# Optimization experiments

Hardware: AMD Instinct MI355X
Metric: run time of the kernel (lower is better)

## Reference

```python
import jax, jax.numpy as jnp
import numpy as np

EMBED_DIM = 32
HIDDEN_DIM = 16

def _xavier(key, fan_in, fan_out):
    limit = float(np.sqrt(6.0 / (fan_in + fan_out)))
    return jax.random.uniform(key, (fan_in, fan_out), jnp.float32, -limit, limit)

def setup_inputs() -> dict:
    key = jax.random.key(0)
    ks = jax.random.split(key, 7)
    N = 1_000_000
    H = jax.random.normal(ks[0], (N, EMBED_DIM), jnp.float32)
    TPL = jax.random.normal(ks[1], (1, 1), jnp.float32)
    # params (xavier-uniform weights, zero biases, matching torch init)
    Wv = _xavier(ks[2], EMBED_DIM, HIDDEN_DIM); bv = jnp.zeros((HIDDEN_DIM,), jnp.float32)
    Wu = _xavier(ks[3], EMBED_DIM, HIDDEN_DIM); bu = jnp.zeros((HIDDEN_DIM,), jnp.float32)
    Ww = _xavier(ks[4], HIDDEN_DIM, 1);        bw = jnp.zeros((1,), jnp.float32)
    W1 = _xavier(ks[5], EMBED_DIM + 1, HIDDEN_DIM); b1 = jnp.zeros((HIDDEN_DIM,), jnp.float32)
    W2 = _xavier(ks[6], HIDDEN_DIM, 1);        b2 = jnp.zeros((1,), jnp.float32)
    return {"H": H, "TPL": TPL, "Wv": Wv, "bv": bv, "Wu": Wu, "bu": bu,
            "Ww": Ww, "bw": bw, "W1": W1, "b1": b1, "W2": W2, "b2": b2}

def reference(H, TPL, Wv, bv, Wu, bu, Ww, bw, W1, b1, W2, b2):
    # Gated attention: V (tanh branch) * U (sigmoid branch); dropout off (eval mode)
    V = jnp.tanh(H @ Wv + bv)                       # (N, hid)
    U = jax.nn.sigmoid(H @ Wu + bu)                 # (N, hid)
    G = V * U                                       # (N, hid)
    A_raw = G @ Ww + bw                             # (N, 1)
    alpha = jax.nn.softmax(A_raw.T, axis=1)         # (1, N)
    B = alpha @ H                                   # (1, D) attention-pooled bag rep
    B_fused = jnp.concatenate([B, TPL], axis=1)     # (1, D+1)
    h = jax.nn.relu(B_fused @ W1 + b1)              # (1, hid)
    score = h @ W2 + b2                             # (1, 1)
    return (score, alpha)
```

## Files before the change

### kernel.cpp

```cpp
#include <hip/hip_runtime.h>

#define NBLK   1024
#define TPB    256
#define D      32
#define HID    16
#define CHUNK  16
#define NWAVES (NBLK * (TPB / 64))

typedef __bf16 bf16x8  __attribute__((ext_vector_type(8)));
typedef float  floatx4 __attribute__((ext_vector_type(4)));

__global__ __launch_bounds__(TPB, 4)
void k1_logits(const float* __restrict__ H,
               const float* __restrict__ Wv, const float* __restrict__ bv,
               const float* __restrict__ Wu, const float* __restrict__ bu,
               const float* __restrict__ Ww, const float* __restrict__ bw,
               float* __restrict__ eout,
               float* __restrict__ partials,
               int N)
{
    __shared__ float ldsE[TPB / 64][16];
    __shared__ float red[TPB / 64][D + 1];

    const int tid  = threadIdx.x;
    const int wave = tid >> 6;
    const int lane = tid & 63;
    const int q    = lane >> 4;
    const int n    = lane & 15;

    bf16x8 bV, bU;
    #pragma unroll
    for (int j = 0; j < 8; ++j) {
        bV[j] = (__bf16)Wv[(q * 8 + j) * HID + n];
        bU[j] = (__bf16)Wu[(q * 8 + j) * HID + n];
    }
    const float bvn = bv[n], bun = bu[n], wwn = Ww[n], bw0 = bw[0];

    float vec[8];
    #pragma unroll
    for (int j = 0; j < 8; ++j) vec[j] = 0.0f;
    float s_acc = 0.0f;

    const int nchunk = N / CHUNK;
    int c = blockIdx.x * (TPB / 64) + wave;

    const float* base0 = H + (size_t)n * D + q * 8;

    float4 pre0, pre1;
    bool has = (c < nchunk);
    if (has) {
        const float* p = base0 + (size_t)c * CHUNK * D;
        pre0 = *reinterpret_cast<const float4*>(p);
        pre1 = *reinterpret_cast<const float4*>(p + 4);
    }

    while (has) {
        const int cn = c + NWAVES;
        const bool hn = (cn < nchunk);
        float4 nxt0, nxt1;
        if (hn) {
            const float* p = base0 + (size_t)cn * CHUNK * D;
            nxt0 = *reinterpret_cast<const float4*>(p);
            nxt1 = *reinterpret_cast<const float4*>(p + 4);
        }

        bf16x8 a;
        a[0] = (__bf16)pre0.x; a[1] = (__bf16)pre0.y;
        a[2] = (__bf16)pre0.z; a[3] = (__bf16)pre0.w;
        a[4] = (__bf16)pre1.x; a[5] = (__bf16)pre1.y;
        a[6] = (__bf16)pre1.z; a[7] = (__bf16)pre1.w;

        floatx4 accV = {0.f, 0.f, 0.f, 0.f};
        floatx4 accU = {0.f, 0.f, 0.f, 0.f};
        accV = __builtin_amdgcn_mfma_f32_16x16x32_bf16(a, bV, accV, 0, 0, 0);
        accU = __builtin_amdgcn_mfma_f32_16x16x32_bf16(a, bU, accU, 0, 0, 0);

        float g[4];
        #pragma unroll
        for (int r = 0; r < 4; ++r) {
            const float v  = accV[r] + bvn;
            const float u  = accU[r] + bun;
            const float th = 1.0f - 2.0f / (__expf(2.0f * v) + 1.0f);
            const float sg = 1.0f / (1.0f + __expf(-u));
            g[r] = th * sg * wwn;
        }
        #pragma unroll
        for (int r = 0; r < 4; ++r) {
            g[r] += __shfl_xor(g[r], 1);
            g[r] += __shfl_xor(g[r], 2);
            g[r] += __shfl_xor(g[r], 4);
            g[r] += __shfl_xor(g[r], 8);
        }
        float4 e4;
        e4.x = __expf(g[0] + bw0);
        e4.y = __expf(g[1] + bw0);
        e4.z = __expf(g[2] + bw0);
        e4.w = __expf(g[3] + bw0);
        if (n == 0) *reinterpret_cast<float4*>(&ldsE[wave][q * 4]) = e4;
        const float em = ldsE[wave][n];
        if (lane < 16) eout[(size_t)c * CHUNK + lane] = em;
        s_acc += em;
        vec[0] = fmaf(em, pre0.x, vec[0]);
        vec[1] = fmaf(em, pre0.y, vec[1]);
        vec[2] = fmaf(em, pre0.z, vec[2]);
        vec[3] = fmaf(em, pre0.w, vec[3]);
        vec[4] = fmaf(em, pre1.x, vec[4]);
        vec[5] = fmaf(em, pre1.y, vec[5]);
        vec[6] = fmaf(em, pre1.z, vec[6]);
        vec[7] = fmaf(em, pre1.w, vec[7]);

        pre0 = nxt0; pre1 = nxt1;
        c = cn;
        has = hn;
    }

    #pragma unroll
    for (int m = 1; m <= 32; m <<= 1) s_acc += __shfl_xor(s_acc, m);
    #pragma unroll
    for (int j = 0; j < 8; ++j) {
        vec[j] += __shfl_xor(vec[j], 1);
        vec[j] += __shfl_xor(vec[j], 2);
        vec[j] += __shfl_xor(vec[j], 4);
        vec[j] += __shfl_xor(vec[j], 8);
    }
    if (lane == 0) red[wave][0] = 0.25f * s_acc;
    if (n == 0) {
        #pragma unroll
        for (int j = 0; j < 8; ++j) red[wave][1 + q * 8 + j] = vec[j];
    }
    __syncthreads();
    if (tid < D + 1) {
        float p = red[0][tid] + red[1][tid] + red[2][tid] + red[3][tid];
        partials[(size_t)tid * NBLK + blockIdx.x] = p;
    }
}

__global__ __launch_bounds__(TPB)
void k2a_reduce(const float* __restrict__ partials,
                double* __restrict__ tot,
                float* __restrict__ scalars)
{
    const int j = blockIdx.x, t = threadIdx.x;
    const float4 v = reinterpret_cast<const float4*>(partials + (size_t)j * NBLK)[t];
    double a = (double)v.x + (double)v.y + (double)v.z + (double)v.w;
    #pragma unroll
    for (int m = 1; m <= 32; m <<= 1) a += __shfl_xor(a, m);
    __shared__ double r[TPB / 64];
    if ((t & 63) == 0) r[t >> 6] = a;
    __syncthreads();
    if (t == 0) {
        const double s = r[0] + r[1] + r[2] + r[3];
        tot[j] = s;
        if (j == 0) scalars[0] = (float)(1.0 / s);
    }
}

__global__ __launch_bounds__(TPB)
void k3_alpha(float* __restrict__ alpha,
              const float* __restrict__ scalars,
              const double* __restrict__ tot,
              const float* __restrict__ TPL,
              const float* __restrict__ W1, const float* __restrict__ b1,
              const float* __restrict__ W2, const float* __restrict__ b2,
              float* __restrict__ score_out, int N)
{
    const float invS = scalars[0];
    const int i4 = blockIdx.x * TPB + threadIdx.x;
    const int n4 = (N - 3) >> 2;
    if (i4 < n4) {
        float4* p = reinterpret_cast<float4*>(alpha + 3) + i4;
        float4 v = *p;
        v.x *= invS; v.y *= invS; v.z *= invS; v.w *= invS;
        *p = v;
    } else if (i4 == n4) {
        alpha[0] *= invS; alpha[1] *= invS; alpha[2] *= invS;
        for (int r = 3 + 4 * n4; r < N; ++r) alpha[r] *= invS;
    }
    if (blockIdx.x == 0 && threadIdx.x < HID) {
        const int t = threadIdx.x;
        float hj = b1[t];
        #pragma unroll
        for (int k = 0; k < D; ++k)
            hj = fmaf((float)(tot[1 + k] * (double)invS), W1[k * HID + t], hj);
        hj = fmaf(TPL[0], W1[D * HID + t], hj);
        hj = fmaxf(hj, 0.0f);
        float pre = hj * W2[t];
        pre += __shfl_xor(pre, 1);
        pre += __shfl_xor(pre, 2);
        pre += __shfl_xor(pre, 4);
        pre += __shfl_xor(pre, 8);
        if (t == 0) score_out[0] = pre + b2[0];
    }
}

extern "C" void kernel_launch(void* const* d_in, const int* in_sizes, int n_in,
                              void* d_out, int out_size, void* d_ws, size_t ws_size,
                              hipStream_t stream) {
    const float* H   = (const float*)d_in[0];
    const float* TPL = (const float*)d_in[1];
    const float* Wv  = (const float*)d_in[2];
    const float* bv  = (const float*)d_in[3];
    const float* Wu  = (const float*)d_in[4];
    const float* bu  = (const float*)d_in[5];
    const float* Ww  = (const float*)d_in[6];
    const float* bw  = (const float*)d_in[7];
    const float* W1  = (const float*)d_in[8];
    const float* b1  = (const float*)d_in[9];
    const float* W2  = (const float*)d_in[10];
    const float* b2  = (const float*)d_in[11];

    float* out = (float*)d_out;
    const int N = in_sizes[0] / D;

    float*  ws_f     = (float*)d_ws;
    float*  partials = ws_f;
    double* tot      = (double*)(ws_f + (size_t)(D + 1) * NBLK);
    float*  scalars  = ws_f + (size_t)(D + 1) * NBLK + 2 * (D + 1) + 2;

    k1_logits<<<NBLK, TPB, 0, stream>>>(H, Wv, bv, Wu, bu, Ww, bw,
                                        out + 1, partials, N);
    k2a_reduce<<<D + 1, TPB, 0, stream>>>(partials, tot, scalars);
    const int n4 = (N - 3) >> 2;
    k3_alpha<<<(n4 + 1 + TPB - 1) / TPB, TPB, 0, stream>>>(out + 1, scalars, tot,
                                                           TPL, W1, b1, W2, b2, out, N);
}
```

Baseline: 211.2 us.

## Swap MFMA operands so rows land per lane, removing LDS exchange and shuffles

Transposes the MFMA product by putting the weights in the A operand and the H rows in the B operand. The output tile then holds hidden units along the row dimension and samples along lanes, so each lane reduces its four hidden values locally with only two cross-row shuffles. This removes the 16 xor-shuffles, the LDS store/load round trip for the exp values, and the redundant exp computations per chunk. Bias and weight vectors are now loaded per row group (four values per lane) instead of per column.

```diff
diff --git a/kernel.cpp b/kernel.cpp
--- a/kernel.cpp
+++ b/kernel.cpp
@@ -19,7 +19,6 @@
                float* __restrict__ partials,
                int N)
 {
-    __shared__ float ldsE[TPB / 64][16];
     __shared__ float red[TPB / 64][D + 1];
 
     const int tid  = threadIdx.x;
@@ -28,13 +27,20 @@
     const int q    = lane >> 4;
     const int n    = lane & 15;
 
-    bf16x8 bV, bU;
+    bf16x8 aV, aU;
     #pragma unroll
     for (int j = 0; j < 8; ++j) {
-        bV[j] = (__bf16)Wv[(q * 8 + j) * HID + n];
-        bU[j] = (__bf16)Wu[(q * 8 + j) * HID + n];
-    }
-    const float bvn = bv[n], bun = bu[n], wwn = Ww[n], bw0 = bw[0];
+        aV[j] = (__bf16)Wv[(q * 8 + j) * HID + n];
+        aU[j] = (__bf16)Wu[(q * 8 + j) * HID + n];
+    }
+    float bv4[4], bu4[4], ww4[4];
+    #pragma unroll
+    for (int r = 0; r < 4; ++r) {
+        bv4[r] = bv[4 * q + r];
+        bu4[r] = bu[4 * q + r];
+        ww4[r] = Ww[4 * q + r];
+    }
+    const float bw0 = bw[0];
 
     float vec[8];
     #pragma unroll
@@ -64,50 +70,39 @@
             nxt1 = *reinterpret_cast<const float4*>(p + 4);
         }
 
-        bf16x8 a;
-        a[0] = (__bf16)pre0.x; a[1] = (__bf16)pre0.y;
-        a[2] = (__bf16)pre0.z; a[3] = (__bf16)pre0.w;
-        a[4] = (__bf16)pre1.x; a[5] = (__bf16)pre1.y;
-        a[6] = (__bf16)pre1.z; a[7] = (__bf16)pre1.w;
+        bf16x8 b;
+        b[0] = (__bf16)pre0.x; b[1] = (__bf16)pre0.y;
+        b[2] = (__bf16)pre0.z; b[3] = (__bf16)pre0.w;
+        b[4] = (__bf16)pre1.x; b[5] = (__bf16)pre1.y;
+        b[6] = (__bf16)pre1.z; b[7] = (__bf16)pre1.w;
 
         floatx4 accV = {0.f, 0.f, 0.f, 0.f};
         floatx4 accU = {0.f, 0.f, 0.f, 0.f};
-        accV = __builtin_amdgcn_mfma_f32_16x16x32_bf16(a, bV, accV, 0, 0, 0);
-        accU = __builtin_amdgcn_mfma_f32_16x16x32_bf16(a, bU, accU, 0, 0, 0);
-
-        float g[4];
+        accV = __builtin_amdgcn_mfma_f32_16x16x32_bf16(aV, b, accV, 0, 0, 0);
+        accU = __builtin_amdgcn_mfma_f32_16x16x32_bf16(aU, b, accU, 0, 0, 0);
+
+        float gl = 0.0f;
         #pragma unroll
         for (int r = 0; r < 4; ++r) {
-            const float v  = accV[r] + bvn;
-            const float u  = accU[r] + bun;
+            const float v  = accV[r] + bv4[r];
+            const float u  = accU[r] + bu4[r];
             const float th = 1.0f - 2.0f / (__expf(2.0f * v) + 1.0f);
             const float sg = 1.0f / (1.0f + __expf(-u));
-            g[r] = th * sg * wwn;
+            gl = fmaf(th * sg, ww4[r], gl);
         }
-        #pragma unroll
-        for (int r = 0; r < 4; ++r) {
-            g[r] += __shfl_xor(g[r], 1);
-            g[r] += __shfl_xor(g[r], 2);
-            g[r] += __shfl_xor(g[r], 4);
-            g[r] += __shfl_xor(g[r], 8);
-        }
-        float4 e4;
-        e4.x = __expf(g[0] + bw0);
-        e4.y = __expf(g[1] + bw0);
-        e4.z = __expf(g[2] + bw0);
-        e4.w = __expf(g[3] + bw0);
-        if (n == 0) *reinterpret_cast<float4*>(&ldsE[wave][q * 4]) = e4;
-        const float em = ldsE[wave][n];
-        if (lane < 16) eout[(size_t)c * CHUNK + lane] = em;
-        s_acc += em;
-        vec[0] = fmaf(em, pre0.x, vec[0]);
-        vec[1] = fmaf(em, pre0.y, vec[1]);
-        vec[2] = fmaf(em, pre0.z, vec[2]);
-        vec[3] = fmaf(em, pre0.w, vec[3]);
-        vec[4] = fmaf(em, pre1.x, vec[4]);
-        vec[5] = fmaf(em, pre1.y, vec[5]);
-        vec[6] = fmaf(em, pre1.z, vec[6]);
-        vec[7] = fmaf(em, pre1.w, vec[7]);
+        gl += __shfl_xor(gl, 16);
+        gl += __shfl_xor(gl, 32);
+        const float e = __expf(gl + bw0);
+        if (lane < 16) eout[(size_t)c * CHUNK + lane] = e;
+        s_acc += e;
+        vec[0] = fmaf(e, pre0.x, vec[0]);
+        vec[1] = fmaf(e, pre0.y, vec[1]);
+        vec[2] = fmaf(e, pre0.z, vec[2]);
+        vec[3] = fmaf(e, pre0.w, vec[3]);
+        vec[4] = fmaf(e, pre1.x, vec[4]);
+        vec[5] = fmaf(e, pre1.y, vec[5]);
+        vec[6] = fmaf(e, pre1.z, vec[6]);
+        vec[7] = fmaf(e, pre1.w, vec[7]);
 
         pre0 = nxt0; pre1 = nxt1;
         c = cn;
```

Result: no change. 209.7 us (-0.7%).
